# Optimization experiments

Measured on AMD Instinct MI355X. Metric: run time of the kernel, lower is better.

The kernel has to match this reference:

```python
import jax, jax.numpy as jnp
import numpy as np

N_SAMPLES = 9
N_FEATURES = 8
GRID_DIM = 200
H, W = 512, 512


def _corner_shifts():
    # same ordering as the torch module: i (x) outer, j (y), k (z) inner
    return jnp.array([[i, j, k] for i in (0, 1) for j in (0, 1) for k in (0, 1)], dtype=jnp.int32)


def setup_inputs() -> dict:
    key = jax.random.key(0)
    k1, k2, k3, k4 = jax.random.split(key, 4)
    b = 1
    vpoints = jax.random.uniform(k1, (b, H * W, 3), jnp.float32, 0.0, float(GRID_DIM))
    veye = jax.random.uniform(k2, (b, 3), jnp.float32, -float(GRID_DIM), 0.0)
    depth = jax.random.uniform(k3, (b, H, W), jnp.float32)
    grid = jax.random.normal(k4, (GRID_DIM, GRID_DIM, GRID_DIM, N_FEATURES), jnp.float32)
    empty_value = jnp.zeros((N_FEATURES,), jnp.float32)
    return {"vpoints": vpoints, "veye": veye, "depth": depth, "grid": grid, "empty_value": empty_value}


def _forward(vpoints, veye, depth, grid, empty_value):
    b, h, w = depth.shape
    # --- create_canonical_view: n_samples points along each viewing ray, centered on vpoints ---
    dirs = vpoints - veye[:, None, :]                                   # (b, n, 3)
    dirs = dirs / jnp.linalg.norm(dirs, axis=-1, keepdims=True)
    offs = jnp.arange(N_SAMPLES, dtype=vpoints.dtype) - (N_SAMPLES // 2)
    cv = vpoints[:, :, None, :] + offs[None, None, :, None] * dirs[:, :, None, :]  # (b, n, s, 3)
    points_normalized = cv - (jnp.floor(cv) + 0.5)

    pts = cv.reshape(-1, 3)  # b == 1 (original squeezes the batch dim); N = n*s
    xs, ys, zs, nf = grid.shape
    valid = ((pts[:, 0] >= 0) & (pts[:, 0] < xs)
             & (pts[:, 1] >= 0) & (pts[:, 1] < ys)
             & (pts[:, 2] >= 0) & (pts[:, 2] < zs))

    # replication-pad volume by 1 voxel; coords shifted by +1 into padded frame
    gp = jnp.pad(grid, ((1, 1), (1, 1), (1, 1), (0, 0)), mode="edge")
    p = jnp.where(valid[:, None], pts, 0.0) + 1.0   # invalid points mapped to a safe in-bounds index
    fl = jnp.floor(p)
    df = p - fl                                      # (N, 3) fractional offsets
    base = fl.astype(jnp.int32)
    idx = base[:, None, :] + _corner_shifts()[None]  # (N, 8, 3)

    corners = gp[idx[..., 0], idx[..., 1], idx[..., 2], :]  # (N, 8, nf) gather

    # trilinear weights, ordering matches corner shift ordering (4i + 2j + k)
    wx = jnp.stack([1.0 - df[:, 0], df[:, 0]], axis=1)
    wy = jnp.stack([1.0 - df[:, 1], df[:, 1]], axis=1)
    wz = jnp.stack([1.0 - df[:, 2], df[:, 2]], axis=1)
    wgt = (wx[:, :, None, None] * wy[:, None, :, None] * wz[:, None, None, :]).reshape(-1, 8)

    interp = jnp.einsum("nc,ncf->nf", wgt, corners)              # (N, nf)
    feats = jnp.where(valid[:, None], interp, empty_value[None, :])

    values = feats.reshape(b, h, w, N_SAMPLES * N_FEATURES)
    values = jnp.transpose(values, (0, 3, 1, 2))                 # (b, s*nf, h, w)
    return values, points_normalized, dirs


def reference(vpoints, veye, depth, grid, empty_value):
    return _forward(vpoints, veye, depth, grid, empty_value)
```

## Files before the change

### kernel.cpp

```cpp
#include <hip/hip_runtime.h>

#define HW (512 * 512)
#define GD 200
#define NS 9
#define NF 8
#define NPB 64
#define BT (NPB * NS)

__global__ __launch_bounds__(BT) void fusion_gather_kernel(
    const float* __restrict__ vpoints,
    const float* __restrict__ veye,
    const float* __restrict__ grid,
    const float* __restrict__ empty_value,
    float* __restrict__ out_values,
    float* __restrict__ out_pn,
    float* __restrict__ out_dirs)
{
    __shared__ float vp[NPB * 3];
    __shared__ float pnbuf[NPB * NS * 3];
    __shared__ float dirbuf[NPB * 3];
    __shared__ float vbuf[NS * NF * 65];

    int tid = threadIdx.x;
    int n0 = blockIdx.x * NPB;

    if (tid < NPB * 3) vp[tid] = vpoints[(size_t)n0 * 3 + tid];
    __syncthreads();

    int r = tid / NS;
    int s = tid - r * NS;

    float px = vp[r * 3 + 0];
    float py = vp[r * 3 + 1];
    float pz = vp[r * 3 + 2];
    float ex = veye[0], ey = veye[1], ez = veye[2];

    float dx = px - ex, dy = py - ey, dz = pz - ez;
    float inv = 1.0f / sqrtf(dx * dx + dy * dy + dz * dz);
    dx *= inv; dy *= inv; dz *= inv;

    if (s == 0) {
        dirbuf[r * 3 + 0] = dx;
        dirbuf[r * 3 + 1] = dy;
        dirbuf[r * 3 + 2] = dz;
    }

    float off = (float)(s - NS / 2);
    float cx = px + off * dx;
    float cy = py + off * dy;
    float cz = pz + off * dz;

    pnbuf[r * 27 + s * 3 + 0] = cx - (floorf(cx) + 0.5f);
    pnbuf[r * 27 + s * 3 + 1] = cy - (floorf(cy) + 0.5f);
    pnbuf[r * 27 + s * 3 + 2] = cz - (floorf(cz) + 0.5f);

    bool valid = (cx >= 0.0f) && (cx < (float)GD) &&
                 (cy >= 0.0f) && (cy < (float)GD) &&
                 (cz >= 0.0f) && (cz < (float)GD);

    float p0 = cx + 1.0f, p1 = cy + 1.0f, p2 = cz + 1.0f;
    float f0 = floorf(p0), f1 = floorf(p1), f2 = floorf(p2);
    float d0 = p0 - f0, d1 = p1 - f1, d2 = p2 - f2;
    int bx = (int)f0, by = (int)f1, bz = (int)f2;
    int X0 = min(max(bx - 1, 0), GD - 1), X1 = min(max(bx, 0), GD - 1);
    int Y0 = min(max(by - 1, 0), GD - 1), Y1 = min(max(by, 0), GD - 1);
    int Z0 = min(max(bz - 1, 0), GD - 1), Z1 = min(max(bz, 0), GD - 1);

    const float4* __restrict__ g4 = (const float4*)grid;

    int col[4];
    col[0] = (X0 * GD + Y0) * GD;
    col[1] = (X0 * GD + Y1) * GD;
    col[2] = (X1 * GD + Y0) * GD;
    col[3] = (X1 * GD + Y1) * GD;

    float4 c[16];
#pragma unroll
    for (int q = 0; q < 4; ++q) {
        c[q * 4 + 0] = g4[(size_t)(col[q] + Z0) * 2 + 0];
        c[q * 4 + 1] = g4[(size_t)(col[q] + Z0) * 2 + 1];
        c[q * 4 + 2] = g4[(size_t)(col[q] + Z1) * 2 + 0];
        c[q * 4 + 3] = g4[(size_t)(col[q] + Z1) * 2 + 1];
    }

    float wx0 = 1.0f - d0, wx1 = d0;
    float wy0 = 1.0f - d1, wy1 = d1;
    float wz0 = 1.0f - d2, wz1 = d2;
    float wq[4];
    wq[0] = wx0 * wy0; wq[1] = wx0 * wy1; wq[2] = wx1 * wy0; wq[3] = wx1 * wy1;

    float acc[NF];
#pragma unroll
    for (int f = 0; f < NF; ++f) acc[f] = 0.0f;

#pragma unroll
    for (int q = 0; q < 4; ++q) {
        float w0 = wq[q] * wz0, w1 = wq[q] * wz1;
        acc[0] += w0 * c[q * 4 + 0].x + w1 * c[q * 4 + 2].x;
        acc[1] += w0 * c[q * 4 + 0].y + w1 * c[q * 4 + 2].y;
        acc[2] += w0 * c[q * 4 + 0].z + w1 * c[q * 4 + 2].z;
        acc[3] += w0 * c[q * 4 + 0].w + w1 * c[q * 4 + 2].w;
        acc[4] += w0 * c[q * 4 + 1].x + w1 * c[q * 4 + 3].x;
        acc[5] += w0 * c[q * 4 + 1].y + w1 * c[q * 4 + 3].y;
        acc[6] += w0 * c[q * 4 + 1].z + w1 * c[q * 4 + 3].z;
        acc[7] += w0 * c[q * 4 + 1].w + w1 * c[q * 4 + 3].w;
    }

    float ev[NF];
#pragma unroll
    for (int f = 0; f < NF; ++f) ev[f] = empty_value[f];

#pragma unroll
    for (int f = 0; f < NF; ++f)
        vbuf[(s * NF + f) * 65 + r] = valid ? acc[f] : ev[f];

    __syncthreads();

    {
        int col_ = tid & 63;
        int w = tid >> 6;
#pragma unroll
        for (int k = 0; k < 8; ++k) {
            int row = w + k * NS;
            __builtin_nontemporal_store(vbuf[row * 65 + col_],
                                        &out_values[(size_t)row * HW + n0 + col_]);
        }
    }
    const size_t pn_base = (size_t)n0 * (NS * 3);
#pragma unroll
    for (int k = 0; k < 3; ++k) {
        int idx = tid + k * BT;
        __builtin_nontemporal_store(pnbuf[idx], &out_pn[pn_base + idx]);
    }
    if (tid < NPB * 3)
        __builtin_nontemporal_store(dirbuf[tid], &out_dirs[(size_t)n0 * 3 + tid]);
}

extern "C" void kernel_launch(void* const* d_in, const int* in_sizes, int n_in,
                              void* d_out, int out_size, void* d_ws, size_t ws_size,
                              hipStream_t stream) {
    const float* vpoints = (const float*)d_in[0];
    const float* veye = (const float*)d_in[1];
    const float* grid = (const float*)d_in[3];
    const float* empty_value = (const float*)d_in[4];

    float* out = (float*)d_out;
    float* out_values = out;
    float* out_pn = out + (size_t)NS * NF * HW;
    float* out_dirs = out_pn + (size_t)HW * NS * 3;

    dim3 block(BT);
    dim3 grid_dim(HW / NPB);
    hipLaunchKernelGGL(fusion_gather_kernel, grid_dim, block, 0, stream,
                       vpoints, veye, grid, empty_value,
                       out_values, out_pn, out_dirs);
}
```

Before: 158.1 us.

## Coarsen threads to two ray samples each and drop vpoint shared staging

The block shrinks from 576 to 320 threads. Five threads now share each point and each thread computes two samples, issuing 32 independent float4 gathers instead of 16 to raise memory-level parallelism. Each thread reads vpoints directly, which removes the shared staging buffer and one barrier. The fifth thread of each point computes sample 8 twice, adding redundant gather work. The doubled corner arrays raise register pressure and may lower occupancy.

New measurement: 228.0 us. 44.2% more time.

```diff
diff --git a/kernel.cpp b/kernel.cpp
--- a/kernel.cpp
+++ b/kernel.cpp
@@ -5,7 +5,7 @@
 #define NS 9
 #define NF 8
 #define NPB 64
-#define BT (NPB * NS)
+#define BT 320
 
 __global__ __launch_bounds__(BT) void fusion_gather_kernel(
     const float* __restrict__ vpoints,
@@ -16,121 +16,156 @@
     float* __restrict__ out_pn,
     float* __restrict__ out_dirs)
 {
-    __shared__ float vp[NPB * 3];
-    __shared__ float pnbuf[NPB * NS * 3];
+    __shared__ float vbuf[NS * NF * 65];
+    __shared__ float pnbuf[NPB * 27];
     __shared__ float dirbuf[NPB * 3];
-    __shared__ float vbuf[NS * NF * 65];
 
     int tid = threadIdx.x;
+    int r = tid / 5;
+    int k = tid - r * 5;
     int n0 = blockIdx.x * NPB;
+    int n = n0 + r;
 
-    if (tid < NPB * 3) vp[tid] = vpoints[(size_t)n0 * 3 + tid];
-    __syncthreads();
-
-    int r = tid / NS;
-    int s = tid - r * NS;
-
-    float px = vp[r * 3 + 0];
-    float py = vp[r * 3 + 1];
-    float pz = vp[r * 3 + 2];
+    float px = vpoints[n * 3 + 0];
+    float py = vpoints[n * 3 + 1];
+    float pz = vpoints[n * 3 + 2];
     float ex = veye[0], ey = veye[1], ez = veye[2];
 
     float dx = px - ex, dy = py - ey, dz = pz - ez;
     float inv = 1.0f / sqrtf(dx * dx + dy * dy + dz * dz);
     dx *= inv; dy *= inv; dz *= inv;
 
-    if (s == 0) {
+    if (k == 0) {
         dirbuf[r * 3 + 0] = dx;
         dirbuf[r * 3 + 1] = dy;
         dirbuf[r * 3 + 2] = dz;
     }
 
-    float off = (float)(s - NS / 2);
-    float cx = px + off * dx;
-    float cy = py + off * dy;
-    float cz = pz + off * dz;
-
-    pnbuf[r * 27 + s * 3 + 0] = cx - (floorf(cx) + 0.5f);
-    pnbuf[r * 27 + s * 3 + 1] = cy - (floorf(cy) + 0.5f);
-    pnbuf[r * 27 + s * 3 + 2] = cz - (floorf(cz) + 0.5f);
-
-    bool valid = (cx >= 0.0f) && (cx < (float)GD) &&
-                 (cy >= 0.0f) && (cy < (float)GD) &&
-                 (cz >= 0.0f) && (cz < (float)GD);
-
-    float p0 = cx + 1.0f, p1 = cy + 1.0f, p2 = cz + 1.0f;
-    float f0 = floorf(p0), f1 = floorf(p1), f2 = floorf(p2);
-    float d0 = p0 - f0, d1 = p1 - f1, d2 = p2 - f2;
-    int bx = (int)f0, by = (int)f1, bz = (int)f2;
-    int X0 = min(max(bx - 1, 0), GD - 1), X1 = min(max(bx, 0), GD - 1);
-    int Y0 = min(max(by - 1, 0), GD - 1), Y1 = min(max(by, 0), GD - 1);
-    int Z0 = min(max(bz - 1, 0), GD - 1), Z1 = min(max(bz, 0), GD - 1);
+    int sA = (k < 4) ? 2 * k : 8;
+    int sB = (k < 4) ? 2 * k + 1 : 8;
 
     const float4* __restrict__ g4 = (const float4*)grid;
 
-    int col[4];
-    col[0] = (X0 * GD + Y0) * GD;
-    col[1] = (X0 * GD + Y1) * GD;
-    col[2] = (X1 * GD + Y0) * GD;
-    col[3] = (X1 * GD + Y1) * GD;
+    float cxA = px + (float)(sA - 4) * dx, cyA = py + (float)(sA - 4) * dy, czA = pz + (float)(sA - 4) * dz;
+    float cxB = px + (float)(sB - 4) * dx, cyB = py + (float)(sB - 4) * dy, czB = pz + (float)(sB - 4) * dz;
 
-    float4 c[16];
+    pnbuf[r * 27 + sA * 3 + 0] = cxA - (floorf(cxA) + 0.5f);
+    pnbuf[r * 27 + sA * 3 + 1] = cyA - (floorf(cyA) + 0.5f);
+    pnbuf[r * 27 + sA * 3 + 2] = czA - (floorf(czA) + 0.5f);
+    pnbuf[r * 27 + sB * 3 + 0] = cxB - (floorf(cxB) + 0.5f);
+    pnbuf[r * 27 + sB * 3 + 1] = cyB - (floorf(cyB) + 0.5f);
+    pnbuf[r * 27 + sB * 3 + 2] = czB - (floorf(czB) + 0.5f);
+
+    bool vA = (cxA >= 0.0f) && (cxA < (float)GD) && (cyA >= 0.0f) && (cyA < (float)GD) &&
+              (czA >= 0.0f) && (czA < (float)GD);
+    bool vB = (cxB >= 0.0f) && (cxB < (float)GD) && (cyB >= 0.0f) && (cyB < (float)GD) &&
+              (czB >= 0.0f) && (czB < (float)GD);
+
+    float pA0 = cxA + 1.0f, pA1 = cyA + 1.0f, pA2 = czA + 1.0f;
+    float fA0 = floorf(pA0), fA1 = floorf(pA1), fA2 = floorf(pA2);
+    float dA0 = pA0 - fA0, dA1 = pA1 - fA1, dA2 = pA2 - fA2;
+    int bxA = (int)fA0, byA = (int)fA1, bzA = (int)fA2;
+    int XA0 = min(max(bxA - 1, 0), GD - 1), XA1 = min(max(bxA, 0), GD - 1);
+    int YA0 = min(max(byA - 1, 0), GD - 1), YA1 = min(max(byA, 0), GD - 1);
+    int ZA0 = min(max(bzA - 1, 0), GD - 1), ZA1 = min(max(bzA, 0), GD - 1);
+
+    float pB0 = cxB + 1.0f, pB1 = cyB + 1.0f, pB2 = czB + 1.0f;
+    float fB0 = floorf(pB0), fB1 = floorf(pB1), fB2 = floorf(pB2);
+    float dB0 = pB0 - fB0, dB1 = pB1 - fB1, dB2 = pB2 - fB2;
+    int bxB = (int)fB0, byB = (int)fB1, bzB = (int)fB2;
+    int XB0 = min(max(bxB - 1, 0), GD - 1), XB1 = min(max(bxB, 0), GD - 1);
+    int YB0 = min(max(byB - 1, 0), GD - 1), YB1 = min(max(byB, 0), GD - 1);
+    int ZB0 = min(max(bzB - 1, 0), GD - 1), ZB1 = min(max(bzB, 0), GD - 1);
+
+    int colA[4], colB[4];
+    colA[0] = (XA0 * GD + YA0) * GD; colA[1] = (XA0 * GD + YA1) * GD;
+    colA[2] = (XA1 * GD + YA0) * GD; colA[3] = (XA1 * GD + YA1) * GD;
+    colB[0] = (XB0 * GD + YB0) * GD; colB[1] = (XB0 * GD + YB1) * GD;
+    colB[2] = (XB1 * GD + YB0) * GD; colB[3] = (XB1 * GD + YB1) * GD;
+
+    float4 cA[16], cB[16];
 #pragma unroll
     for (int q = 0; q < 4; ++q) {
-        c[q * 4 + 0] = g4[(size_t)(col[q] + Z0) * 2 + 0];
-        c[q * 4 + 1] = g4[(size_t)(col[q] + Z0) * 2 + 1];
-        c[q * 4 + 2] = g4[(size_t)(col[q] + Z1) * 2 + 0];
-        c[q * 4 + 3] = g4[(size_t)(col[q] + Z1) * 2 + 1];
+        cA[q * 4 + 0] = g4[(size_t)(colA[q] + ZA0) * 2 + 0];
+        cA[q * 4 + 1] = g4[(size_t)(colA[q] + ZA0) * 2 + 1];
+        cA[q * 4 + 2] = g4[(size_t)(colA[q] + ZA1) * 2 + 0];
+        cA[q * 4 + 3] = g4[(size_t)(colA[q] + ZA1) * 2 + 1];
     }
-
-    float wx0 = 1.0f - d0, wx1 = d0;
-    float wy0 = 1.0f - d1, wy1 = d1;
-    float wz0 = 1.0f - d2, wz1 = d2;
-    float wq[4];
-    wq[0] = wx0 * wy0; wq[1] = wx0 * wy1; wq[2] = wx1 * wy0; wq[3] = wx1 * wy1;
-
-    float acc[NF];
-#pragma unroll
-    for (int f = 0; f < NF; ++f) acc[f] = 0.0f;
-
 #pragma unroll
     for (int q = 0; q < 4; ++q) {
-        float w0 = wq[q] * wz0, w1 = wq[q] * wz1;
-        acc[0] += w0 * c[q * 4 + 0].x + w1 * c[q * 4 + 2].x;
-        acc[1] += w0 * c[q * 4 + 0].y + w1 * c[q * 4 + 2].y;
-        acc[2] += w0 * c[q * 4 + 0].z + w1 * c[q * 4 + 2].z;
-        acc[3] += w0 * c[q * 4 + 0].w + w1 * c[q * 4 + 2].w;
-        acc[4] += w0 * c[q * 4 + 1].x + w1 * c[q * 4 + 3].x;
-        acc[5] += w0 * c[q * 4 + 1].y + w1 * c[q * 4 + 3].y;
-        acc[6] += w0 * c[q * 4 + 1].z + w1 * c[q * 4 + 3].z;
-        acc[7] += w0 * c[q * 4 + 1].w + w1 * c[q * 4 + 3].w;
+        cB[q * 4 + 0] = g4[(size_t)(colB[q] + ZB0) * 2 + 0];
+        cB[q * 4 + 1] = g4[(size_t)(colB[q] + ZB0) * 2 + 1];
+        cB[q * 4 + 2] = g4[(size_t)(colB[q] + ZB1) * 2 + 0];
+        cB[q * 4 + 3] = g4[(size_t)(colB[q] + ZB1) * 2 + 1];
     }
 
     float ev[NF];
 #pragma unroll
     for (int f = 0; f < NF; ++f) ev[f] = empty_value[f];
 
+    {
+        float wx0 = 1.0f - dA0, wy0 = 1.0f - dA1, wz0 = 1.0f - dA2;
+        float wq[4] = {wx0 * wy0, wx0 * dA1, dA0 * wy0, dA0 * dA1};
+        float acc[NF];
 #pragma unroll
-    for (int f = 0; f < NF; ++f)
-        vbuf[(s * NF + f) * 65 + r] = valid ? acc[f] : ev[f];
+        for (int f = 0; f < NF; ++f) acc[f] = 0.0f;
+#pragma unroll
+        for (int q = 0; q < 4; ++q) {
+            float w0 = wq[q] * wz0, w1 = wq[q] * dA2;
+            acc[0] += w0 * cA[q * 4 + 0].x + w1 * cA[q * 4 + 2].x;
+            acc[1] += w0 * cA[q * 4 + 0].y + w1 * cA[q * 4 + 2].y;
+            acc[2] += w0 * cA[q * 4 + 0].z + w1 * cA[q * 4 + 2].z;
+            acc[3] += w0 * cA[q * 4 + 0].w + w1 * cA[q * 4 + 2].w;
+            acc[4] += w0 * cA[q * 4 + 1].x + w1 * cA[q * 4 + 3].x;
+            acc[5] += w0 * cA[q * 4 + 1].y + w1 * cA[q * 4 + 3].y;
+            acc[6] += w0 * cA[q * 4 + 1].z + w1 * cA[q * 4 + 3].z;
+            acc[7] += w0 * cA[q * 4 + 1].w + w1 * cA[q * 4 + 3].w;
+        }
+#pragma unroll
+        for (int f = 0; f < NF; ++f)
+            vbuf[(sA * NF + f) * 65 + r] = vA ? acc[f] : ev[f];
+    }
+
+    {
+        float wx0 = 1.0f - dB0, wy0 = 1.0f - dB1, wz0 = 1.0f - dB2;
+        float wq[4] = {wx0 * wy0, wx0 * dB1, dB0 * wy0, dB0 * dB1};
+        float acc[NF];
+#pragma unroll
+        for (int f = 0; f < NF; ++f) acc[f] = 0.0f;
+#pragma unroll
+        for (int q = 0; q < 4; ++q) {
+            float w0 = wq[q] * wz0, w1 = wq[q] * dB2;
+            acc[0] += w0 * cB[q * 4 + 0].x + w1 * cB[q * 4 + 2].x;
+            acc[1] += w0 * cB[q * 4 + 0].y + w1 * cB[q * 4 + 2].y;
+            acc[2] += w0 * cB[q * 4 + 0].z + w1 * cB[q * 4 + 2].z;
+            acc[3] += w0 * cB[q * 4 + 0].w + w1 * cB[q * 4 + 2].w;
+            acc[4] += w0 * cB[q * 4 + 1].x + w1 * cB[q * 4 + 3].x;
+            acc[5] += w0 * cB[q * 4 + 1].y + w1 * cB[q * 4 + 3].y;
+            acc[6] += w0 * cB[q * 4 + 1].z + w1 * cB[q * 4 + 3].z;
+            acc[7] += w0 * cB[q * 4 + 1].w + w1 * cB[q * 4 + 3].w;
+        }
+#pragma unroll
+        for (int f = 0; f < NF; ++f)
+            vbuf[(sB * NF + f) * 65 + r] = vB ? acc[f] : ev[f];
+    }
 
     __syncthreads();
 
-    {
-        int col_ = tid & 63;
-        int w = tid >> 6;
 #pragma unroll
-        for (int k = 0; k < 8; ++k) {
-            int row = w + k * NS;
-            __builtin_nontemporal_store(vbuf[row * 65 + col_],
-                                        &out_values[(size_t)row * HW + n0 + col_]);
+    for (int j = 0; j < 15; ++j) {
+        int idx = tid + j * BT;
+        if (idx < NS * NF * 64) {
+            int row = idx >> 6, col = idx & 63;
+            __builtin_nontemporal_store(vbuf[row * 65 + col],
+                                        &out_values[(size_t)row * HW + n0 + col]);
         }
     }
-    const size_t pn_base = (size_t)n0 * (NS * 3);
+    const size_t pn_base = (size_t)n0 * 27;
 #pragma unroll
-    for (int k = 0; k < 3; ++k) {
-        int idx = tid + k * BT;
-        __builtin_nontemporal_store(pnbuf[idx], &out_pn[pn_base + idx]);
+    for (int j = 0; j < 6; ++j) {
+        int idx = tid + j * BT;
+        if (idx < NPB * 27)
+            __builtin_nontemporal_store(pnbuf[idx], &out_pn[pn_base + idx]);
     }
     if (tid < NPB * 3)
         __builtin_nontemporal_store(dirbuf[tid], &out_dirs[(size_t)n0 * 3 + tid]);
```
